# Optimization experiments

Hardware: AMD Instinct MI355X
Metric: run time of the kernel (lower is better)

Reference implementation:

```python
import jax, jax.numpy as jnp
import numpy as np
from jax import lax

CTX = 768  # ctx_len from the module globals


def _causal_grouped_conv(sig, w):
    # sig: [B,C,L], w: [C,K] -> [B,C,L]; torch F.conv1d(groups=C) with left pad K-1
    # (cross-correlation semantics, same as lax.conv_general_dilated)
    K = w.shape[-1]
    return lax.conv_general_dilated(
        sig, w[:, None, :], (1,), [(K - 1, 0)],
        feature_group_count=sig.shape[1],
        dimension_numbers=("NCH", "OIH", "NCH"))


def setup_inputs() -> dict:
    key = jax.random.key(0)
    ks = jax.random.split(key, 10)
    B, T, C = 8, 767, 1024
    s = 1.0 / np.sqrt(C).astype(np.float32)
    return {
        "x": jax.random.normal(ks[0], (B, T, C), jnp.float32),
        "xx": jax.random.normal(ks[1], (B, C), jnp.float32),          # prev-token state
        "aa": jax.random.uniform(ks[2], (B, C), jnp.float32),          # wkv numerator carry
        "bb": jax.random.uniform(ks[3], (B, C), jnp.float32) + 0.5,    # wkv denominator carry (>0)
        "mm": jnp.zeros((B, C), jnp.float32),                          # prev power-of-two normalizer (log-ish)
        "time_decay": jax.random.normal(ks[4], (C, 1), jnp.float32) * 0.1,
        "time_first": jnp.full((C, 1), np.log(0.3), jnp.float32),
        "time_mix": jax.random.uniform(ks[5], (1, 1, C), jnp.float32),
        "Wk": jax.random.normal(ks[6], (C, C), jnp.float32) * s,
        "Wv": jax.random.normal(ks[7], (C, C), jnp.float32) * s,
        "Wr": jax.random.normal(ks[8], (C, C), jnp.float32) * s,
        "Wo": jax.random.normal(ks[9], (C, C), jnp.float32) * s,
    }


def reference(x, xx, aa, bb, mm, time_decay, time_first, time_mix, Wk, Wv, Wr, Wo):
    B, T, C = x.shape
    # time_shift: prepend carried last-token features, drop last
    x_prev = jnp.concatenate([xx[:, None, :], x[:, :-1, :]], axis=1)
    xm = x * time_mix + x_prev * (1.0 - time_mix)
    k = jnp.einsum('btc,dc->bdt', xm, Wk)  # [B,C,T]
    v = jnp.einsum('btc,dc->bdt', xm, Wv)
    r = jnp.einsum('btc,dc->btd', xm, Wr)  # [B,T,C]
    # power-of-two normalizer via frexp/ldexp (no grad path, exponent is int)
    m = jnp.max(k, axis=-1)                                  # [B,C]
    _, expn = jnp.frexp(lax.stop_gradient(m))
    mm_new = jnp.ldexp(jnp.asarray(0.5, k.dtype), expn)      # 0.5 * 2**exp
    k = jnp.exp(k - mm_new[..., None])
    kv = k * v
    # decay kernel: time_curve = [-(CTX-2)..0], last column = exp(time_first)
    time_curve = -(CTX - 2.0 - jnp.arange(CTX - 1, dtype=x.dtype))
    w_full = jnp.exp(jnp.concatenate(
        [jnp.exp(time_decay) * time_curve[None, :], time_first], axis=-1))  # [C,CTX]
    # carry-in columns rescaled to new normalizer
    rsf = jnp.exp(mm - mm_new)                               # [B,C]
    k_ext = jnp.concatenate([(bb * rsf)[..., None], k], axis=-1)    # [B,C,T+1]
    kv_ext = jnp.concatenate([(aa * rsf)[..., None], kv], axis=-1)  # [B,C,T+1]
    w = w_full[:, -(T + 1):]                                 # [C,T+1]
    wkv = _causal_grouped_conv(kv_ext, w)[..., 1:]           # [B,C,T]
    wk = _causal_grouped_conv(k_ext, w)[..., 1:]             # [B,C,T]
    rwkv = jax.nn.sigmoid(r) * jnp.nan_to_num(wkv / wk).transpose(0, 2, 1)  # [B,T,C]
    return jnp.einsum('btc,dc->btd', rwkv, Wo)
```

## Files before the change

kernel.cpp:

```cpp
#include <hip/hip_runtime.h>
#include <float.h>


typedef __bf16 bf16x8 __attribute__((ext_vector_type(8)));
typedef __bf16 bf16x4 __attribute__((ext_vector_type(4)));
typedef float  f32x4  __attribute__((ext_vector_type(4)));

#define NCH 16

#define GLOAD_LDS16(g, l)                                                  \
  __builtin_amdgcn_global_load_lds(                                       \
      (__attribute__((address_space(1))) void*)(g),                       \
      (__attribute__((address_space(3))) void*)(l), 16, 0, 0)

__global__ __launch_bounds__(256)
void xm_split_kernel(const float* __restrict__ x, const float* __restrict__ xx,
                     const float* __restrict__ tmix,
                     __bf16* __restrict__ xh, __bf16* __restrict__ xl,
                     int B, int T, int C, int Mpad) {
  long i4 = (long)blockIdx.x * 256 + threadIdx.x;
  long tot = (long)Mpad * C / 4;
  if (i4 >= tot) return;
  long flat = i4 * 4;
  int c = (int)(flat % C);
  long m = flat / C;
  float4 o;
  if (m >= (long)B * T) {
    o = make_float4(0.f, 0.f, 0.f, 0.f);
  } else {
    int t = (int)(m % T);
    int b = (int)(m / T);
    float4 xv = *(const float4*)&x[flat];
    float4 tm = *(const float4*)&tmix[c];
    float4 pv;
    if (t == 0) pv = *(const float4*)&xx[(long)b * C + c];
    else        pv = *(const float4*)&x[flat - C];
    o.x = xv.x * tm.x + pv.x * (1.0f - tm.x);
    o.y = xv.y * tm.y + pv.y * (1.0f - tm.y);
    o.z = xv.z * tm.z + pv.z * (1.0f - tm.z);
    o.w = xv.w * tm.w + pv.w * (1.0f - tm.w);
  }
  bf16x4 hv, lv;
  hv[0] = (__bf16)o.x; lv[0] = (__bf16)(o.x - (float)hv[0]);
  hv[1] = (__bf16)o.y; lv[1] = (__bf16)(o.y - (float)hv[1]);
  hv[2] = (__bf16)o.z; lv[2] = (__bf16)(o.z - (float)hv[2]);
  hv[3] = (__bf16)o.w; lv[3] = (__bf16)(o.w - (float)hv[3]);
  *(bf16x4*)&xh[flat] = hv;
  *(bf16x4*)&xl[flat] = lv;
}

__global__ __launch_bounds__(256)
void w_split_kernel(const float* __restrict__ W0, const float* __restrict__ W1,
                    const float* __restrict__ W2, const float* __restrict__ W3,
                    __bf16* __restrict__ wh, __bf16* __restrict__ wl, long CC) {
  int z = blockIdx.y;
  const float* __restrict__ W = (z == 0) ? W0 : (z == 1) ? W1 : (z == 2) ? W2 : W3;
  long i4 = (long)blockIdx.x * 256 + threadIdx.x;
  if (i4 * 4 >= CC) return;
  long flat = i4 * 4;
  float4 v = *(const float4*)&W[flat];
  bf16x4 hv, lv;
  hv[0] = (__bf16)v.x; lv[0] = (__bf16)(v.x - (float)hv[0]);
  hv[1] = (__bf16)v.y; lv[1] = (__bf16)(v.y - (float)hv[1]);
  hv[2] = (__bf16)v.z; lv[2] = (__bf16)(v.z - (float)hv[2]);
  hv[3] = (__bf16)v.w; lv[3] = (__bf16)(v.w - (float)hv[3]);
  *(bf16x4*)&wh[z * CC + flat] = hv;
  *(bf16x4*)&wl[z * CC + flat] = lv;
}

__global__ __launch_bounds__(256)
void gemm_split(const __bf16* __restrict__ Xh, const __bf16* __restrict__ Xl,
                const __bf16* __restrict__ Wh, const __bf16* __restrict__ Wl,
                float* __restrict__ O0, float* __restrict__ O1,
                float* __restrict__ O2, int M, int N, int K) {
  const int z = blockIdx.z;
  const __bf16* __restrict__ Bh = Wh + (size_t)z * N * K;
  const __bf16* __restrict__ Bl = Wl + (size_t)z * N * K;
  float* __restrict__ O = (z == 0) ? O0 : (z == 1) ? O1 : O2;

  __shared__ __bf16 sAh[128 * 32];
  __shared__ __bf16 sAl[128 * 32];
  __shared__ __bf16 sBh[128 * 32];
  __shared__ __bf16 sBl[128 * 32];

  const int tid  = threadIdx.x;
  const int wid  = tid >> 6;
  const int lane = tid & 63;
  const int bm = blockIdx.x * 128;
  const int bn = blockIdx.y * 128;
  const int wrow = wid >> 1;
  const int wcol = wid & 1;

  f32x4 acc[4][4] = {};

  const int srow = lane >> 2;
  const int scu  = lane & 3;

  for (int k0 = 0; k0 < K; k0 += 32) {
    __syncthreads();
    #pragma unroll
    for (int i = 0; i < 2; ++i) {
      const int rb0 = wid * 32 + i * 16;
      const size_t ga = (size_t)(bm + rb0 + srow) * K + k0 + scu * 8;
      const size_t gb = (size_t)(bn + rb0 + srow) * K + k0 + scu * 8;
      const int lo = rb0 * 32;
      GLOAD_LDS16(&Xh[ga], &sAh[lo]);
      GLOAD_LDS16(&Xl[ga], &sAl[lo]);
      GLOAD_LDS16(&Bh[gb], &sBh[lo]);
      GLOAD_LDS16(&Bl[gb], &sBl[lo]);
    }
    __syncthreads();

    const int lrow = lane & 15;
    const int lk   = (lane >> 4) * 8;
    bf16x8 ah[4], al[4], bh[4], bl[4];
    #pragma unroll
    for (int m = 0; m < 4; ++m) {
      const int r = (wrow * 64 + m * 16 + lrow) * 32 + lk;
      ah[m] = *(const bf16x8*)&sAh[r];
      al[m] = *(const bf16x8*)&sAl[r];
    }
    #pragma unroll
    for (int n = 0; n < 4; ++n) {
      const int r = (wcol * 64 + n * 16 + lrow) * 32 + lk;
      bh[n] = *(const bf16x8*)&sBh[r];
      bl[n] = *(const bf16x8*)&sBl[r];
    }
    #pragma unroll
    for (int m = 0; m < 4; ++m)
      #pragma unroll
      for (int n = 0; n < 4; ++n) {
        acc[m][n] = __builtin_amdgcn_mfma_f32_16x16x32_bf16(ah[m], bh[n], acc[m][n], 0, 0, 0);
        acc[m][n] = __builtin_amdgcn_mfma_f32_16x16x32_bf16(ah[m], bl[n], acc[m][n], 0, 0, 0);
        acc[m][n] = __builtin_amdgcn_mfma_f32_16x16x32_bf16(al[m], bh[n], acc[m][n], 0, 0, 0);
      }
  }

  const int crow = (lane >> 4) * 4;
  const int ccol = lane & 15;
  #pragma unroll
  for (int m = 0; m < 4; ++m)
    #pragma unroll
    for (int n = 0; n < 4; ++n) {
      const int gn = bn + wcol * 64 + n * 16 + ccol;
      #pragma unroll
      for (int i = 0; i < 4; ++i) {
        const int gm = bm + wrow * 64 + m * 16 + crow + i;
        if (gm < M) O[(size_t)gm * N + gn] = acc[m][n][i];
      }
    }
}

__global__ __launch_bounds__(256)
void scan_pass1(const float* __restrict__ kbuf, const float* __restrict__ vbuf,
                const float* __restrict__ td,
                float* __restrict__ P, float* __restrict__ Skv,
                float* __restrict__ Sk, int B, int T, int C, int L) {
  int g = blockIdx.x * 256 + threadIdx.x;
  int j = blockIdx.y;
  int b = g / C, c = g % C;
  float decay = expf(-expf(td[c]));
  int t0 = j * L, t1 = min(T, t0 + L);
  float skv = 0.0f, sk = 0.0f, p = 1.0f;
  size_t base = (size_t)b * T * C + c;
  #pragma unroll 4
  for (int t = t0; t < t1; ++t) {
    size_t idx = base + (size_t)t * C;
    float kk = expf(kbuf[idx]);
    float kv = kk * vbuf[idx];
    skv = fmaf(decay, skv, kv);
    sk  = fmaf(decay, sk, kk);
    p *= decay;
  }
  size_t o = (size_t)j * (B * C) + g;
  P[o] = p; Skv[o] = skv; Sk[o] = sk;
}

__global__ __launch_bounds__(256)
void scan_combine(const float* __restrict__ P, const float* __restrict__ Skv,
                  const float* __restrict__ Sk, const float* __restrict__ aa,
                  const float* __restrict__ bb, const float* __restrict__ mm,
                  float* __restrict__ A0kv, float* __restrict__ A0k, int BC) {
  int g = blockIdx.x * 256 + threadIdx.x;
  if (g >= BC) return;
  float rsf = expf(mm[g]);
  float A = aa[g] * rsf;
  float Bst = bb[g] * rsf;
  #pragma unroll
  for (int j = 0; j < NCH; ++j) {
    size_t o = (size_t)j * BC + g;
    float p = P[o], skv = Skv[o], sk = Sk[o];
    A0kv[o] = A; A0k[o] = Bst;
    A   = fmaf(p, A, skv);
    Bst = fmaf(p, Bst, sk);
  }
}

__global__ __launch_bounds__(256)
void scan_pass2(const float* __restrict__ kbuf, const float* __restrict__ vbuf,
                const float* __restrict__ rbuf, const float* __restrict__ td,
                const float* __restrict__ tf, const float* __restrict__ A0kv,
                const float* __restrict__ A0k,
                __bf16* __restrict__ oh, __bf16* __restrict__ ol,
                int B, int T, int C, int L) {
  int g = blockIdx.x * 256 + threadIdx.x;
  int j = blockIdx.y;
  int b = g / C, c = g % C;
  float decay = expf(-expf(td[c]));
  float tfe = expf(tf[c]);
  size_t o = (size_t)j * (B * C) + g;
  float A = A0kv[o];
  float Bst = A0k[o];
  int t0 = j * L, t1 = min(T, t0 + L);
  size_t base = (size_t)b * T * C + c;
  #pragma unroll 4
  for (int t = t0; t < t1; ++t) {
    size_t idx = base + (size_t)t * C;
    float kr = kbuf[idx];
    float vv = vbuf[idx];
    float rr = rbuf[idx];
    float kk = expf(kr);
    float kv = kk * vv;
    float wkv = fmaf(kv, tfe, A);
    float wk  = fmaf(kk, tfe, Bst);
    float q = wkv / wk;
    if (isnan(q)) q = 0.0f;
    else if (isinf(q)) q = (q > 0.0f) ? FLT_MAX : -FLT_MAX;
    float sig = 1.0f / (1.0f + expf(-rr));
    float val = sig * q;
    __bf16 h = (__bf16)val;
    oh[idx] = h;
    ol[idx] = (__bf16)(val - (float)h);
    A   = fmaf(decay, A, kv);
    Bst = fmaf(decay, Bst, kk);
  }
}

extern "C" void kernel_launch(void* const* d_in, const int* in_sizes, int n_in,
                              void* d_out, int out_size, void* d_ws, size_t ws_size,
                              hipStream_t stream) {
  const float* x    = (const float*)d_in[0];
  const float* xx   = (const float*)d_in[1];
  const float* aa   = (const float*)d_in[2];
  const float* bb   = (const float*)d_in[3];
  const float* mm   = (const float*)d_in[4];
  const float* td   = (const float*)d_in[5];
  const float* tf   = (const float*)d_in[6];
  const float* tmix = (const float*)d_in[7];
  const float* Wk   = (const float*)d_in[8];
  const float* Wv   = (const float*)d_in[9];
  const float* Wr   = (const float*)d_in[10];
  const float* Wo   = (const float*)d_in[11];
  float* out = (float*)d_out;

  const int C = in_sizes[5];
  const int B = in_sizes[1] / C;
  const int T = in_sizes[0] / (B * C);
  const int M = B * T;
  const int Mpad = ((M + 127) / 128) * 128;
  const int BC = B * C;
  const long CC = (long)C * C;
  const int L = (T + NCH - 1) / NCH;

  char* p = (char*)d_ws;
  __bf16* xh = (__bf16*)p;  p += (size_t)Mpad * C * 2;
  __bf16* xl = (__bf16*)p;  p += (size_t)Mpad * C * 2;
  __bf16* wh = (__bf16*)p;  p += (size_t)4 * CC * 2;
  __bf16* wl = (__bf16*)p;  p += (size_t)4 * CC * 2;
  float* kb  = (float*)p;   p += (size_t)M * C * 4;
  float* vb  = (float*)p;   p += (size_t)M * C * 4;
  float* rb  = (float*)p;   p += (size_t)M * C * 4;
  float* Pb   = (float*)(wh);
  float* Skv  = (float*)(wh + CC);
  float* Sk   = (float*)(wh + 2 * CC);
  float* A0kv = (float*)(wl);
  float* A0k  = (float*)(wl + CC);
  __bf16* rh = xh;
  __bf16* rl = xl;

  long nf4 = (long)Mpad * C / 4;
  xm_split_kernel<<<dim3((unsigned)((nf4 + 255) / 256)), 256, 0, stream>>>(
      x, xx, tmix, xh, xl, B, T, C, Mpad);

  w_split_kernel<<<dim3((unsigned)(CC / 4 / 256), 4), 256, 0, stream>>>(
      Wk, Wv, Wr, Wo, wh, wl, CC);

  dim3 g3(Mpad / 128, C / 128, 3);
  gemm_split<<<g3, 256, 0, stream>>>(xh, xl, wh, wl, kb, vb, rb, M, C, C);

  scan_pass1<<<dim3(BC / 256, NCH), 256, 0, stream>>>(kb, vb, td, Pb, Skv, Sk,
                                                      B, T, C, L);
  scan_combine<<<dim3(BC / 256), 256, 0, stream>>>(Pb, Skv, Sk, aa, bb, mm,
                                                   A0kv, A0k, BC);
  scan_pass2<<<dim3(BC / 256, NCH), 256, 0, stream>>>(kb, vb, rb, td, tf,
                                                      A0kv, A0k, rh, rl,
                                                      B, T, C, L);

  dim3 g1(Mpad / 128, C / 128, 1);
  gemm_split<<<g1, 256, 0, stream>>>(rh, rl, wh + 3 * CC, wl + 3 * CC,
                                     out, out, out, M, C, C);
}
```

Before: 313.3 us.

## Use 32x32 MFMA tiles, double scan chunks, cache exp(k) and k*v in pass1

The split-bf16 GEMM switches from 16x16x32 to 32x32x16 MFMA with 2x2 accumulator tiles per wave, which needs fewer LDS fragment loads per MFMA. The scan chunk count goes from 16 to 32 for more parallelism. Pass1 now writes exp(k) and k*v back into the k/v buffers so pass2 skips the exp recompute, at the cost of extra global writes. The chunk decay product is computed in closed form as exp(-etd*len).

```diff
diff --git a/kernel.cpp b/kernel.cpp
--- a/kernel.cpp
+++ b/kernel.cpp
@@ -4,9 +4,9 @@
 
 typedef __bf16 bf16x8 __attribute__((ext_vector_type(8)));
 typedef __bf16 bf16x4 __attribute__((ext_vector_type(4)));
-typedef float  f32x4  __attribute__((ext_vector_type(4)));
-
-#define NCH 16
+typedef float  f32x16 __attribute__((ext_vector_type(16)));
+
+#define NCH 32
 
 #define GLOAD_LDS16(g, l)                                                  \
   __builtin_amdgcn_global_load_lds(                                       \
@@ -91,7 +91,7 @@
   const int wrow = wid >> 1;
   const int wcol = wid & 1;
 
-  f32x4 acc[4][4] = {};
+  f32x16 acc[2][2] = {};
 
   const int srow = lane >> 2;
   const int scu  = lane & 3;
@@ -111,69 +111,79 @@
     }
     __syncthreads();
 
-    const int lrow = lane & 15;
-    const int lk   = (lane >> 4) * 8;
-    bf16x8 ah[4], al[4], bh[4], bl[4];
-    #pragma unroll
-    for (int m = 0; m < 4; ++m) {
-      const int r = (wrow * 64 + m * 16 + lrow) * 32 + lk;
-      ah[m] = *(const bf16x8*)&sAh[r];
-      al[m] = *(const bf16x8*)&sAl[r];
-    }
-    #pragma unroll
-    for (int n = 0; n < 4; ++n) {
-      const int r = (wcol * 64 + n * 16 + lrow) * 32 + lk;
-      bh[n] = *(const bf16x8*)&sBh[r];
-      bl[n] = *(const bf16x8*)&sBl[r];
-    }
-    #pragma unroll
-    for (int m = 0; m < 4; ++m)
+    const int frow = lane & 31;
+    const int fk   = (lane >> 5) * 8;
+    bf16x8 ah[2][2], al[2][2], bh[2][2], bl[2][2];
+    #pragma unroll
+    for (int m = 0; m < 2; ++m)
       #pragma unroll
-      for (int n = 0; n < 4; ++n) {
-        acc[m][n] = __builtin_amdgcn_mfma_f32_16x16x32_bf16(ah[m], bh[n], acc[m][n], 0, 0, 0);
-        acc[m][n] = __builtin_amdgcn_mfma_f32_16x16x32_bf16(ah[m], bl[n], acc[m][n], 0, 0, 0);
-        acc[m][n] = __builtin_amdgcn_mfma_f32_16x16x32_bf16(al[m], bh[n], acc[m][n], 0, 0, 0);
+      for (int s = 0; s < 2; ++s) {
+        const int r = (wrow * 64 + m * 32 + frow) * 32 + s * 16 + fk;
+        ah[m][s] = *(const bf16x8*)&sAh[r];
+        al[m][s] = *(const bf16x8*)&sAl[r];
       }
-  }
-
-  const int crow = (lane >> 4) * 4;
-  const int ccol = lane & 15;
+    #pragma unroll
+    for (int n = 0; n < 2; ++n)
+      #pragma unroll
+      for (int s = 0; s < 2; ++s) {
+        const int r = (wcol * 64 + n * 32 + frow) * 32 + s * 16 + fk;
+        bh[n][s] = *(const bf16x8*)&sBh[r];
+        bl[n][s] = *(const bf16x8*)&sBl[r];
+      }
+    #pragma unroll
+    for (int m = 0; m < 2; ++m)
+      #pragma unroll
+      for (int n = 0; n < 2; ++n)
+        #pragma unroll
+        for (int s = 0; s < 2; ++s) {
+          acc[m][n] = __builtin_amdgcn_mfma_f32_32x32x16_bf16(ah[m][s], bh[n][s], acc[m][n], 0, 0, 0);
+          acc[m][n] = __builtin_amdgcn_mfma_f32_32x32x16_bf16(ah[m][s], bl[n][s], acc[m][n], 0, 0, 0);
+          acc[m][n] = __builtin_amdgcn_mfma_f32_32x32x16_bf16(al[m][s], bh[n][s], acc[m][n], 0, 0, 0);
+        }
+  }
+
+  const int ccol  = lane & 31;
+  const int rbase = 4 * (lane >> 5);
   #pragma unroll
-  for (int m = 0; m < 4; ++m)
-    #pragma unroll
-    for (int n = 0; n < 4; ++n) {
-      const int gn = bn + wcol * 64 + n * 16 + ccol;
+  for (int m = 0; m < 2; ++m)
+    #pragma unroll
+    for (int n = 0; n < 2; ++n) {
+      const int gn = bn + wcol * 64 + n * 32 + ccol;
       #pragma unroll
-      for (int i = 0; i < 4; ++i) {
-        const int gm = bm + wrow * 64 + m * 16 + crow + i;
-        if (gm < M) O[(size_t)gm * N + gn] = acc[m][n][i];
+      for (int r = 0; r < 16; ++r) {
+        const int row = (r & 3) + 8 * (r >> 2) + rbase;
+        const int gm = bm + wrow * 64 + m * 32 + row;
+        if (gm < M) O[(size_t)gm * N + gn] = acc[m][n][r];
       }
     }
 }
 
 __global__ __launch_bounds__(256)
-void scan_pass1(const float* __restrict__ kbuf, const float* __restrict__ vbuf,
+void scan_pass1(float* __restrict__ kbuf, float* __restrict__ vbuf,
                 const float* __restrict__ td,
                 float* __restrict__ P, float* __restrict__ Skv,
                 float* __restrict__ Sk, int B, int T, int C, int L) {
   int g = blockIdx.x * 256 + threadIdx.x;
   int j = blockIdx.y;
   int b = g / C, c = g % C;
-  float decay = expf(-expf(td[c]));
+  float etd = expf(td[c]);
+  float decay = expf(-etd);
   int t0 = j * L, t1 = min(T, t0 + L);
-  float skv = 0.0f, sk = 0.0f, p = 1.0f;
+  float skv = 0.0f, sk = 0.0f;
   size_t base = (size_t)b * T * C + c;
   #pragma unroll 4
   for (int t = t0; t < t1; ++t) {
     size_t idx = base + (size_t)t * C;
     float kk = expf(kbuf[idx]);
     float kv = kk * vbuf[idx];
+    kbuf[idx] = kk;
+    vbuf[idx] = kv;
     skv = fmaf(decay, skv, kv);
     sk  = fmaf(decay, sk, kk);
-    p *= decay;
   }
   size_t o = (size_t)j * (B * C) + g;
-  P[o] = p; Skv[o] = skv; Sk[o] = sk;
+  P[o] = expf(-etd * (float)(t1 - t0));
+  Skv[o] = skv; Sk[o] = sk;
 }
 
 __global__ __launch_bounds__(256)
@@ -216,11 +226,9 @@
   #pragma unroll 4
   for (int t = t0; t < t1; ++t) {
     size_t idx = base + (size_t)t * C;
-    float kr = kbuf[idx];
-    float vv = vbuf[idx];
+    float kk = kbuf[idx];
+    float kv = vbuf[idx];
     float rr = rbuf[idx];
-    float kk = expf(kr);
-    float kv = kk * vv;
     float wkv = fmaf(kv, tfe, A);
     float wk  = fmaf(kk, tfe, Bst);
     float q = wkv / wk;
```

New measurement: 348.2 us. +11.1%, slower.
